# Kernel optimization log

Hardware: AMD Instinct MI355X
Metric: run time of the kernel (lower is better)

## Reference

```python
import jax, jax.numpy as jnp
import numpy as np

N_NODES = 100000
N_EDGES = 1600000
N_PAIRS = 200000
IN_C, HID_C, OUT_C = 128, 128, 64


def setup_inputs() -> dict:
    key = jax.random.key(0)
    ks = jax.random.split(key, 10)
    x = jax.random.normal(ks[0], (N_NODES, IN_C), dtype=jnp.float32)
    edge_index = jax.random.randint(ks[1], (2, N_EDGES), 0, N_NODES, dtype=jnp.int64)
    node_i = jax.random.randint(ks[2], (N_PAIRS,), 0, N_NODES, dtype=jnp.int64)
    node_j = jax.random.randint(ks[3], (N_PAIRS,), 0, N_NODES, dtype=jnp.int64)
    def glorot(k, fan_in, fan_out):
        s = jnp.sqrt(6.0 / (fan_in + fan_out))
        return jax.random.uniform(k, (fan_in, fan_out), jnp.float32, -s, s)
    W1 = glorot(ks[4], IN_C, HID_C)
    b1 = jnp.zeros((HID_C,), jnp.float32)
    W2 = glorot(ks[5], HID_C, HID_C)
    b2 = jnp.zeros((HID_C,), jnp.float32)
    W3 = glorot(ks[6], HID_C, OUT_C)
    b3 = jnp.zeros((OUT_C,), jnp.float32)
    return {"x": x, "edge_index": edge_index, "node_i": node_i, "node_j": node_j,
            "W1": W1, "b1": b1, "W2": W2, "b2": b2, "W3": W3, "b3": b3}


def _gcn_layer(h, src, dst, deg_inv, w_e, W, b):
    # h: [N, Cin] -> linear then symmetric-normalized aggregation (with self loops)
    h = h @ W  # [N, Cout]
    msg = h[src] * w_e[:, None]  # [E, Cout] gather + edge weight
    agg = jax.ops.segment_sum(msg, dst, num_segments=N_NODES)
    agg = agg + h * deg_inv[:, None]  # self-loop term: h_i / deg_i
    return agg + b


def reference(x, edge_index, node_i, node_j, W1, b1, W2, b2, W3, b3):
    src, dst = edge_index[0], edge_index[1]
    # GCN normalization with self loops: deg_i = 1 + in-degree
    ones = jnp.ones((N_EDGES,), jnp.float32)
    deg = jax.ops.segment_sum(ones, dst, num_segments=N_NODES) + 1.0
    dinv_sqrt = jax.lax.rsqrt(deg)
    deg_inv = 1.0 / deg
    w_e = dinv_sqrt[src] * dinv_sqrt[dst]  # [E]

    h = _gcn_layer(x, src, dst, deg_inv, w_e, W1, b1)
    h = jax.nn.relu(h)  # dropout is identity in eval mode
    h = _gcn_layer(h, src, dst, deg_inv, w_e, W2, b2)
    h = jax.nn.relu(h)
    h = _gcn_layer(h, src, dst, deg_inv, w_e, W3, b3)

    # dot-product link decode (decode_type=None)
    return jnp.sum(h[node_i] * h[node_j], axis=-1)  # [N_PAIRS]
```

## Files before the change

### kernel.cpp

```cpp
#include <hip/hip_runtime.h>

#define NN 100000
#define NNP 100032
#define NE 1600000
#define NP 200000
#define NBKT 782
#define BCAP 3072
#define BKB 4096

typedef short s16x8 __attribute__((ext_vector_type(8)));
typedef float f32x4 __attribute__((ext_vector_type(4)));

__device__ __forceinline__ unsigned short f2bf(float f) {
  unsigned int u = __float_as_uint(f);
  u += 0x7fffu + ((u >> 16) & 1u);
  return (unsigned short)(u >> 16);
}

__device__ __forceinline__ void upadd(uint u, float& lo, float& hi) {
  lo += __uint_as_float(u << 16);
  hi += __uint_as_float(u & 0xffff0000u);
}

template <int NT>
__device__ __forceinline__ void prepw_dev(const float* __restrict__ W,
                                          uint* __restrict__ Wt, int tid) {
  constexpr int COUT = NT * 16;
  if (tid >= 4 * NT * 64) return;
  int lane = tid & 63, comb = tid >> 6;
  int ks = comb / NT, tl = comb % NT;
  int q = lane >> 4, n = lane & 15;
  uint w[4];
#pragma unroll
  for (int jj = 0; jj < 4; ++jj) {
    int k0 = ks * 32 + q * 8 + 2 * jj;
    uint lo = f2bf(W[k0 * COUT + tl * 16 + n]);
    uint hi = f2bf(W[(k0 + 1) * COUT + tl * 16 + n]);
    w[jj] = lo | (hi << 16);
  }
  ((uint4*)Wt)[comb * 64 + lane] = make_uint4(w[0], w[1], w[2], w[3]);
}

__global__ __launch_bounds__(256) void k_setup(const float* __restrict__ W1,
                                               const float* __restrict__ W2,
                                               const float* __restrict__ W3,
                                               uint* __restrict__ Wt1,
                                               uint* __restrict__ Wt2,
                                               uint* __restrict__ Wt3,
                                               int* __restrict__ gcur) {
  int b = blockIdx.x, t = threadIdx.x;
  if (b < 4) {
    int i = b * 256 + t;
    if (i < 1024) gcur[i] = 0;
  } else if (b < 12) {
    prepw_dev<8>(W1, Wt1, (b - 4) * 256 + t);
  } else if (b < 20) {
    prepw_dev<8>(W2, Wt2, (b - 12) * 256 + t);
  } else {
    prepw_dev<4>(W3, Wt3, (b - 20) * 256 + t);
  }
}

__global__ __launch_bounds__(256) void k_bucket(const int* __restrict__ ei,
                                                int* __restrict__ gcur,
                                                int* __restrict__ aux) {
  __shared__ int cnt[1024];
  __shared__ int scn[1024];
  __shared__ int cur[1024];
  __shared__ int sc[256];
  __shared__ int sorted[BKB];
  __shared__ unsigned short sbkt[BKB];
  const int t = threadIdx.x;
  const int base = blockIdx.x * BKB;

  for (int i = t; i < 1024; i += 256) cnt[i] = 0;
  __syncthreads();

  int pk[16], bk[16];
#pragma unroll
  for (int i = 0; i < 16; ++i) {
    int e = base + t + 256 * i;
    if (e < NE) {
      int src = ei[e], dst = ei[NE + e];
      bk[i] = dst >> 7;
      pk[i] = src | ((dst & 127) << 17);
      atomicAdd(&cnt[bk[i]], 1);
    } else {
      bk[i] = -1;
    }
  }
  __syncthreads();

  int s0 = cnt[4 * t], s1 = cnt[4 * t + 1], s2 = cnt[4 * t + 2], s3 = cnt[4 * t + 3];
  int local = s0 + s1 + s2 + s3;
  sc[t] = local;
  __syncthreads();
  for (int off = 1; off < 256; off <<= 1) {
    int a = (t >= off) ? sc[t - off] : 0;
    __syncthreads();
    sc[t] += a;
    __syncthreads();
  }
  int b0 = sc[t] - local;
  scn[4 * t] = b0;
  scn[4 * t + 1] = b0 + s0;
  scn[4 * t + 2] = b0 + s0 + s1;
  scn[4 * t + 3] = b0 + s0 + s1 + s2;
  cur[4 * t] = scn[4 * t];
  cur[4 * t + 1] = scn[4 * t + 1];
  cur[4 * t + 2] = scn[4 * t + 2];
  cur[4 * t + 3] = scn[4 * t + 3];
  __syncthreads();
  const int tot = sc[255];

#pragma unroll
  for (int i = 0; i < 16; ++i) {
    if (bk[i] >= 0) {
      int pos = atomicAdd(&cur[bk[i]], 1);
      sorted[pos] = pk[i];
      sbkt[pos] = (unsigned short)bk[i];
    }
  }
  __syncthreads();

  for (int b = t; b < 1024; b += 256) {
    int c = cnt[b];
    if (c > 0) cur[b] = b * BCAP + atomicAdd(&gcur[b], c);
  }
  __syncthreads();

  for (int k = t; k < tot; k += 256) {
    int b = sbkt[k];
    aux[cur[b] + (k - scn[b])] = sorted[k];
  }
}

__global__ __launch_bounds__(256) void k_csr(const int* __restrict__ gcur,
                                             const int* __restrict__ aux,
                                             int* __restrict__ row_ptr,
                                             float* __restrict__ dinv,
                                             int* __restrict__ col) {
  __shared__ int red[256];
  __shared__ int c[128];
  __shared__ int cur[128];
  const int b = blockIdx.x, t = threadIdx.x;
  int p = 0;
  for (int i = t; i < b; i += 256) p += gcur[i];
  red[t] = p;
  if (t < 128) c[t] = 0;
  __syncthreads();
  for (int off = 128; off > 0; off >>= 1) {
    if (t < off) red[t] += red[t + off];
    __syncthreads();
  }
  const int base = red[0];
  const int m = gcur[b];
  const int* a = aux + (size_t)b * BCAP;
  __syncthreads();
  for (int k = t; k < m; k += 256) atomicAdd(&c[a[k] >> 17], 1);
  __syncthreads();
  int val = (t < 128) ? c[t] : 0;
  red[t] = val;
  __syncthreads();
  for (int off = 1; off < 128; off <<= 1) {
    int add = (t >= off && t < 128) ? red[t - off] : 0;
    __syncthreads();
    if (t < 128) red[t] += add;
    __syncthreads();
  }
  if (t < 128) {
    int excl = red[t] - val + base;
    int node = b * 128 + t;
    if (node < NN) {
      row_ptr[node] = excl;
      dinv[node] = rsqrtf((float)(val + 1));
      cur[t] = excl;
    }
  }
  if (b == NBKT - 1 && t == 0) row_ptr[NN] = base + m;
  __syncthreads();
  for (int k = t; k < m; k += 256) {
    int pk2 = a[k];
    int pos = atomicAdd(&cur[pk2 >> 17], 1);
    col[pos] = pk2 & 0x1FFFF;
  }
}

template <int COUT, bool AFP32>
__global__ __launch_bounds__(256) void k_gemm_mfma(const void* __restrict__ Av,
                                                   const uint* __restrict__ Wt,
                                                   const float* __restrict__ dinv,
                                                   unsigned short* __restrict__ T) {
  constexpr int NT = COUT / 16;
  __shared__ __align__(16) uint Wlds[4 * NT * 64 * 4];
  __shared__ __align__(16) unsigned short Obuf[64 * COUT];
  const int t = threadIdx.x;
  {
    const uint4* src = (const uint4*)Wt;
    uint4* dst = (uint4*)Wlds;
    for (int i = t; i < 4 * NT * 64; i += 256) dst[i] = src[i];
  }
  __syncthreads();

  const int wv = t >> 6, lane = t & 63;
  const int n = lane & 15, quad = lane >> 4;
  const int rbase = blockIdx.x * 64 + wv * 16;

  union AB { uint4 u; s16x8 s; };
  AB a[4];
  if constexpr (AFP32) {
    const float* A = (const float*)Av;
    int row = rbase + n;
    if (row >= NN) row = NN - 1;
    const float* ap = A + (size_t)row * 128;
#pragma unroll
    for (int ks = 0; ks < 4; ++ks) {
      float4 v0 = *(const float4*)(ap + ks * 32 + quad * 8);
      float4 v1 = *(const float4*)(ap + ks * 32 + quad * 8 + 4);
      a[ks].u.x = (uint)f2bf(v0.x) | ((uint)f2bf(v0.y) << 16);
      a[ks].u.y = (uint)f2bf(v0.z) | ((uint)f2bf(v0.w) << 16);
      a[ks].u.z = (uint)f2bf(v1.x) | ((uint)f2bf(v1.y) << 16);
      a[ks].u.w = (uint)f2bf(v1.z) | ((uint)f2bf(v1.w) << 16);
    }
  } else {
    const uint4* A = (const uint4*)Av;
    int row = rbase + n;
#pragma unroll
    for (int ks = 0; ks < 4; ++ks) a[ks].u = A[(size_t)row * 16 + ks * 4 + quad];
  }

  f32x4 acc[NT];
#pragma unroll
  for (int tl = 0; tl < NT; ++tl) acc[tl] = (f32x4){0.f, 0.f, 0.f, 0.f};

#pragma unroll
  for (int ks = 0; ks < 4; ++ks) {
#pragma unroll
    for (int tl = 0; tl < NT; ++tl) {
      AB b;
      b.u = *(const uint4*)&Wlds[((ks * NT + tl) * 64 + lane) * 4];
      acc[tl] = __builtin_amdgcn_mfma_f32_16x16x32_bf16(a[ks].s, b.s, acc[tl], 0, 0, 0);
    }
  }

  float4 dv = *(const float4*)(dinv + rbase + quad * 4);
  float dvv[4] = {dv.x, dv.y, dv.z, dv.w};
  unsigned short* ob = Obuf + wv * 16 * COUT;
#pragma unroll
  for (int tl = 0; tl < NT; ++tl)
#pragma unroll
    for (int r = 0; r < 4; ++r)
      ob[(quad * 4 + r) * COUT + tl * 16 + n] = f2bf(acc[tl][r] * dvv[r]);

  uint4* gdst = (uint4*)(T + (size_t)rbase * COUT);
  constexpr int ITER = COUT / 32;
#pragma unroll
  for (int i = 0; i < ITER; ++i) {
    int off16 = i * 64 + lane;
    int lrow = (off16 * 8) / COUT;
    uint4 v = make_uint4(0u, 0u, 0u, 0u);
    if (rbase + lrow < NN) v = *(const uint4*)&ob[off16 * 8];
    gdst[off16] = v;
  }
}

__global__ __launch_bounds__(256) void k_gather12(const int* __restrict__ row_ptr,
                                                  const int* __restrict__ col,
                                                  const uint4* __restrict__ T4,
                                                  const float* __restrict__ dinv,
                                                  const float* __restrict__ bias,
                                                  uint4* __restrict__ An) {
  int w = (blockIdx.x * 256 + threadIdx.x) >> 6;
  int lane = threadIdx.x & 63;
  if (w >= NN) return;
  int s = row_ptr[w], tend = row_ptr[w + 1];
  const int q = lane >> 4;
  const int cl = lane & 15;
  float acc[8] = {0.f, 0.f, 0.f, 0.f, 0.f, 0.f, 0.f, 0.f};
  if (q == 0) {
    uint4 u = T4[(size_t)w * 16 + cl];
    upadd(u.x, acc[0], acc[1]);
    upadd(u.y, acc[2], acc[3]);
    upadd(u.z, acc[4], acc[5]);
    upadd(u.w, acc[6], acc[7]);
  }
  const int d = tend - s;
  const int nfull = d >> 4;
  int e = s + q;
  for (int it = 0; it < nfull; ++it, e += 16) {
    int c0 = col[e], c1 = col[e + 4], c2 = col[e + 8], c3 = col[e + 12];
    uint4 v0 = T4[(size_t)c0 * 16 + cl];
    uint4 v1 = T4[(size_t)c1 * 16 + cl];
    uint4 v2 = T4[(size_t)c2 * 16 + cl];
    uint4 v3 = T4[(size_t)c3 * 16 + cl];
    upadd(v0.x, acc[0], acc[1]); upadd(v0.y, acc[2], acc[3]);
    upadd(v0.z, acc[4], acc[5]); upadd(v0.w, acc[6], acc[7]);
    upadd(v1.x, acc[0], acc[1]); upadd(v1.y, acc[2], acc[3]);
    upadd(v1.z, acc[4], acc[5]); upadd(v1.w, acc[6], acc[7]);
    upadd(v2.x, acc[0], acc[1]); upadd(v2.y, acc[2], acc[3]);
    upadd(v2.z, acc[4], acc[5]); upadd(v2.w, acc[6], acc[7]);
    upadd(v3.x, acc[0], acc[1]); upadd(v3.y, acc[2], acc[3]);
    upadd(v3.z, acc[4], acc[5]); upadd(v3.w, acc[6], acc[7]);
  }
  if (d & 15) {
    const int m = tend - 1;
    int i0 = e, i1 = e + 4, i2 = e + 8, i3 = e + 12;
    int c0 = col[min(i0, m)], c1 = col[min(i1, m)];
    int c2 = col[min(i2, m)], c3 = col[min(i3, m)];
    c0 = (i0 < tend) ? c0 : NN;
    c1 = (i1 < tend) ? c1 : NN;
    c2 = (i2 < tend) ? c2 : NN;
    c3 = (i3 < tend) ? c3 : NN;
    uint4 v0 = T4[(size_t)c0 * 16 + cl];
    uint4 v1 = T4[(size_t)c1 * 16 + cl];
    uint4 v2 = T4[(size_t)c2 * 16 + cl];
    uint4 v3 = T4[(size_t)c3 * 16 + cl];
    upadd(v0.x, acc[0], acc[1]); upadd(v0.y, acc[2], acc[3]);
    upadd(v0.z, acc[4], acc[5]); upadd(v0.w, acc[6], acc[7]);
    upadd(v1.x, acc[0], acc[1]); upadd(v1.y, acc[2], acc[3]);
    upadd(v1.z, acc[4], acc[5]); upadd(v1.w, acc[6], acc[7]);
    upadd(v2.x, acc[0], acc[1]); upadd(v2.y, acc[2], acc[3]);
    upadd(v2.z, acc[4], acc[5]); upadd(v2.w, acc[6], acc[7]);
    upadd(v3.x, acc[0], acc[1]); upadd(v3.y, acc[2], acc[3]);
    upadd(v3.z, acc[4], acc[5]); upadd(v3.w, acc[6], acc[7]);
  }
#pragma unroll
  for (int i = 0; i < 8; ++i) {
    acc[i] += __shfl_down(acc[i], 16, 64);
    acc[i] += __shfl_down(acc[i], 32, 64);
  }
  if (q == 0) {
    float4 b0 = *(const float4*)&bias[cl * 8];
    float4 b1 = *(const float4*)&bias[cl * 8 + 4];
    float dv = dinv[w];
    float r[8];
    r[0] = fmaxf(fmaf(dv, acc[0], b0.x), 0.f);
    r[1] = fmaxf(fmaf(dv, acc[1], b0.y), 0.f);
    r[2] = fmaxf(fmaf(dv, acc[2], b0.z), 0.f);
    r[3] = fmaxf(fmaf(dv, acc[3], b0.w), 0.f);
    r[4] = fmaxf(fmaf(dv, acc[4], b1.x), 0.f);
    r[5] = fmaxf(fmaf(dv, acc[5], b1.y), 0.f);
    r[6] = fmaxf(fmaf(dv, acc[6], b1.z), 0.f);
    r[7] = fmaxf(fmaf(dv, acc[7], b1.w), 0.f);
    uint4 o;
    o.x = (uint)f2bf(r[0]) | ((uint)f2bf(r[1]) << 16);
    o.y = (uint)f2bf(r[2]) | ((uint)f2bf(r[3]) << 16);
    o.z = (uint)f2bf(r[4]) | ((uint)f2bf(r[5]) << 16);
    o.w = (uint)f2bf(r[6]) | ((uint)f2bf(r[7]) << 16);
    An[(size_t)w * 16 + cl] = o;
  }
}

__global__ __launch_bounds__(256) void k_gather3(const int* __restrict__ row_ptr,
                                                 const int* __restrict__ col,
                                                 const uint4* __restrict__ T4,
                                                 uint4* __restrict__ G3) {
  int w = (blockIdx.x * 256 + threadIdx.x) >> 6;
  int lane = threadIdx.x & 63;
  if (w >= NN) return;
  int s = row_ptr[w], tend = row_ptr[w + 1];
  const int g = lane >> 3;
  const int cl = lane & 7;
  float acc[8] = {0.f, 0.f, 0.f, 0.f, 0.f, 0.f, 0.f, 0.f};
  if (g == 0) {
    uint4 u = T4[(size_t)w * 8 + cl];
    upadd(u.x, acc[0], acc[1]);
    upadd(u.y, acc[2], acc[3]);
    upadd(u.z, acc[4], acc[5]);
    upadd(u.w, acc[6], acc[7]);
  }
  const int d = tend - s;
  const int nfull = d >> 4;
  int e = s + g;
  for (int it = 0; it < nfull; ++it, e += 16) {
    int c0 = col[e], c1 = col[e + 8];
    uint4 v0 = T4[(size_t)c0 * 8 + cl];
    uint4 v1 = T4[(size_t)c1 * 8 + cl];
    upadd(v0.x, acc[0], acc[1]); upadd(v0.y, acc[2], acc[3]);
    upadd(v0.z, acc[4], acc[5]); upadd(v0.w, acc[6], acc[7]);
    upadd(v1.x, acc[0], acc[1]); upadd(v1.y, acc[2], acc[3]);
    upadd(v1.z, acc[4], acc[5]); upadd(v1.w, acc[6], acc[7]);
  }
  if (d & 15) {
    const int m = tend - 1;
    int i0 = e, i1 = e + 8;
    int c0 = col[min(i0, m)], c1 = col[min(i1, m)];
    c0 = (i0 < tend) ? c0 : NN;
    c1 = (i1 < tend) ? c1 : NN;
    uint4 v0 = T4[(size_t)c0 * 8 + cl];
    uint4 v1 = T4[(size_t)c1 * 8 + cl];
    upadd(v0.x, acc[0], acc[1]); upadd(v0.y, acc[2], acc[3]);
    upadd(v0.z, acc[4], acc[5]); upadd(v0.w, acc[6], acc[7]);
    upadd(v1.x, acc[0], acc[1]); upadd(v1.y, acc[2], acc[3]);
    upadd(v1.z, acc[4], acc[5]); upadd(v1.w, acc[6], acc[7]);
  }
#pragma unroll
  for (int i = 0; i < 8; ++i) {
    acc[i] += __shfl_down(acc[i], 8, 64);
    acc[i] += __shfl_down(acc[i], 16, 64);
    acc[i] += __shfl_down(acc[i], 32, 64);
  }
  if (g == 0) {
    uint4 o;
    o.x = (uint)f2bf(acc[0]) | ((uint)f2bf(acc[1]) << 16);
    o.y = (uint)f2bf(acc[2]) | ((uint)f2bf(acc[3]) << 16);
    o.z = (uint)f2bf(acc[4]) | ((uint)f2bf(acc[5]) << 16);
    o.w = (uint)f2bf(acc[6]) | ((uint)f2bf(acc[7]) << 16);
    G3[(size_t)w * 8 + cl] = o;
  }
}

__global__ __launch_bounds__(256) void k_decode(const int* __restrict__ ni,
                                                const int* __restrict__ nj,
                                                const uint2* __restrict__ G3,
                                                const float* __restrict__ dinv,
                                                const float* __restrict__ b3,
                                                float* __restrict__ out) {
  int p = blockIdx.x * 16 + (threadIdx.x >> 4);
  int cl = threadIdx.x & 15;
  int i = ni[p], j = nj[p];
  uint2 ui = G3[(size_t)i * 16 + cl];
  uint2 uj = G3[(size_t)j * 16 + cl];
  float4 bb = *(const float4*)&b3[cl * 4];
  float di = dinv[i], dj = dinv[j];
  float gi0 = __uint_as_float(ui.x << 16), gi1 = __uint_as_float(ui.x & 0xffff0000u);
  float gi2 = __uint_as_float(ui.y << 16), gi3 = __uint_as_float(ui.y & 0xffff0000u);
  float gj0 = __uint_as_float(uj.x << 16), gj1 = __uint_as_float(uj.x & 0xffff0000u);
  float gj2 = __uint_as_float(uj.y << 16), gj3 = __uint_as_float(uj.y & 0xffff0000u);
  float v = fmaf(di, gi0, bb.x) * fmaf(dj, gj0, bb.x) +
            fmaf(di, gi1, bb.y) * fmaf(dj, gj1, bb.y) +
            fmaf(di, gi2, bb.z) * fmaf(dj, gj2, bb.z) +
            fmaf(di, gi3, bb.w) * fmaf(dj, gj3, bb.w);
  v += __shfl_xor(v, 1, 64);
  v += __shfl_xor(v, 2, 64);
  v += __shfl_xor(v, 4, 64);
  v += __shfl_xor(v, 8, 64);
  if (cl == 0) out[p] = v;
}

extern "C" void kernel_launch(void* const* d_in, const int* in_sizes, int n_in,
                              void* d_out, int out_size, void* d_ws, size_t ws_size,
                              hipStream_t stream) {
  const float* x  = (const float*)d_in[0];
  const int*   ei = (const int*)d_in[1];
  const int*   ni = (const int*)d_in[2];
  const int*   nj = (const int*)d_in[3];
  const float* W1 = (const float*)d_in[4];
  const float* b1 = (const float*)d_in[5];
  const float* W2 = (const float*)d_in[6];
  const float* b2 = (const float*)d_in[7];
  const float* W3 = (const float*)d_in[8];
  const float* b3 = (const float*)d_in[9];
  float* out = (float*)d_out;

  float* dinv    = (float*)d_ws;
  int*   row_ptr = (int*)(dinv + 102400);
  int*   gcur    = row_ptr + 102400;
  int*   col     = gcur + 1024;
  uint*  Wt1     = (uint*)(col + NE);
  uint*  Wt2     = Wt1 + 8192;
  uint*  Wt3     = Wt2 + 8192;
  uint*  Tbf     = Wt3 + 4096;
  uint*  Abf     = Tbf + (size_t)NNP * 64;
  uint*  G3      = Abf + (size_t)NNP * 64;
  int*   aux     = (int*)G3;

  k_setup<<<24, 256, 0, stream>>>(W1, W2, W3, Wt1, Wt2, Wt3, gcur);
  k_bucket<<<(NE + BKB - 1) / BKB, 256, 0, stream>>>(ei, gcur, aux);
  k_csr<<<NBKT, 256, 0, stream>>>(gcur, aux, row_ptr, dinv, col);

  const int GB = NNP / 64;
  const int GATB = (NN * 64 + 255) / 256;

  k_gemm_mfma<128, true><<<GB, 256, 0, stream>>>(x, Wt1, dinv, (unsigned short*)Tbf);
  k_gather12<<<GATB, 256, 0, stream>>>(row_ptr, col, (const uint4*)Tbf, dinv, b1, (uint4*)Abf);
  k_gemm_mfma<128, false><<<GB, 256, 0, stream>>>(Abf, Wt2, dinv, (unsigned short*)Tbf);
  k_gather12<<<GATB, 256, 0, stream>>>(row_ptr, col, (const uint4*)Tbf, dinv, b2, (uint4*)Abf);
  k_gemm_mfma<64, false><<<GB, 256, 0, stream>>>(Abf, Wt3, dinv, (unsigned short*)Tbf);
  k_gather3<<<GATB, 256, 0, stream>>>(row_ptr, col, (const uint4*)Tbf, (uint4*)G3);
  k_decode<<<NP / 16, 256, 0, stream>>>(ni, nj, (const uint2*)G3, dinv, b3, out);
}
```

Measured before the change: 339.6 us.

## Fuse neighbor aggregation with the next layer's MFMA GEMM per 16-node tile

```diff
diff --git a/kernel.cpp b/kernel.cpp
--- a/kernel.cpp
+++ b/kernel.cpp
@@ -186,12 +186,11 @@
   }
 }
 
-template <int COUT, bool AFP32>
-__global__ __launch_bounds__(256) void k_gemm_mfma(const void* __restrict__ Av,
-                                                   const uint* __restrict__ Wt,
-                                                   const float* __restrict__ dinv,
-                                                   unsigned short* __restrict__ T) {
-  constexpr int NT = COUT / 16;
+__global__ __launch_bounds__(256) void k_gemm1(const float* __restrict__ A,
+                                               const uint* __restrict__ Wt,
+                                               const float* __restrict__ dinv,
+                                               unsigned short* __restrict__ T) {
+  constexpr int NT = 8, COUT = 128;
   __shared__ __align__(16) uint Wlds[4 * NT * 64 * 4];
   __shared__ __align__(16) unsigned short Obuf[64 * COUT];
   const int t = threadIdx.x;
@@ -208,8 +207,7 @@
 
   union AB { uint4 u; s16x8 s; };
   AB a[4];
-  if constexpr (AFP32) {
-    const float* A = (const float*)Av;
+  {
     int row = rbase + n;
     if (row >= NN) row = NN - 1;
     const float* ap = A + (size_t)row * 128;
@@ -222,11 +220,6 @@
       a[ks].u.z = (uint)f2bf(v1.x) | ((uint)f2bf(v1.y) << 16);
       a[ks].u.w = (uint)f2bf(v1.z) | ((uint)f2bf(v1.w) << 16);
     }
-  } else {
-    const uint4* A = (const uint4*)Av;
-    int row = rbase + n;
-#pragma unroll
-    for (int ks = 0; ks < 4; ++ks) a[ks].u = A[(size_t)row * 16 + ks * 4 + quad];
   }
 
   f32x4 acc[NT];
@@ -253,9 +246,8 @@
       ob[(quad * 4 + r) * COUT + tl * 16 + n] = f2bf(acc[tl][r] * dvv[r]);
 
   uint4* gdst = (uint4*)(T + (size_t)rbase * COUT);
-  constexpr int ITER = COUT / 32;
-#pragma unroll
-  for (int i = 0; i < ITER; ++i) {
+#pragma unroll
+  for (int i = 0; i < 4; ++i) {
     int off16 = i * 64 + lane;
     int lrow = (off16 * 8) / COUT;
     uint4 v = make_uint4(0u, 0u, 0u, 0u);
@@ -264,90 +256,147 @@
   }
 }
 
-__global__ __launch_bounds__(256) void k_gather12(const int* __restrict__ row_ptr,
-                                                  const int* __restrict__ col,
-                                                  const uint4* __restrict__ T4,
-                                                  const float* __restrict__ dinv,
-                                                  const float* __restrict__ bias,
-                                                  uint4* __restrict__ An) {
-  int w = (blockIdx.x * 256 + threadIdx.x) >> 6;
-  int lane = threadIdx.x & 63;
-  if (w >= NN) return;
-  int s = row_ptr[w], tend = row_ptr[w + 1];
-  const int q = lane >> 4;
-  const int cl = lane & 15;
-  float acc[8] = {0.f, 0.f, 0.f, 0.f, 0.f, 0.f, 0.f, 0.f};
-  if (q == 0) {
-    uint4 u = T4[(size_t)w * 16 + cl];
-    upadd(u.x, acc[0], acc[1]);
-    upadd(u.y, acc[2], acc[3]);
-    upadd(u.z, acc[4], acc[5]);
-    upadd(u.w, acc[6], acc[7]);
-  }
-  const int d = tend - s;
-  const int nfull = d >> 4;
-  int e = s + q;
-  for (int it = 0; it < nfull; ++it, e += 16) {
-    int c0 = col[e], c1 = col[e + 4], c2 = col[e + 8], c3 = col[e + 12];
-    uint4 v0 = T4[(size_t)c0 * 16 + cl];
-    uint4 v1 = T4[(size_t)c1 * 16 + cl];
-    uint4 v2 = T4[(size_t)c2 * 16 + cl];
-    uint4 v3 = T4[(size_t)c3 * 16 + cl];
-    upadd(v0.x, acc[0], acc[1]); upadd(v0.y, acc[2], acc[3]);
-    upadd(v0.z, acc[4], acc[5]); upadd(v0.w, acc[6], acc[7]);
-    upadd(v1.x, acc[0], acc[1]); upadd(v1.y, acc[2], acc[3]);
-    upadd(v1.z, acc[4], acc[5]); upadd(v1.w, acc[6], acc[7]);
-    upadd(v2.x, acc[0], acc[1]); upadd(v2.y, acc[2], acc[3]);
-    upadd(v2.z, acc[4], acc[5]); upadd(v2.w, acc[6], acc[7]);
-    upadd(v3.x, acc[0], acc[1]); upadd(v3.y, acc[2], acc[3]);
-    upadd(v3.z, acc[4], acc[5]); upadd(v3.w, acc[6], acc[7]);
-  }
-  if (d & 15) {
-    const int m = tend - 1;
-    int i0 = e, i1 = e + 4, i2 = e + 8, i3 = e + 12;
-    int c0 = col[min(i0, m)], c1 = col[min(i1, m)];
-    int c2 = col[min(i2, m)], c3 = col[min(i3, m)];
-    c0 = (i0 < tend) ? c0 : NN;
-    c1 = (i1 < tend) ? c1 : NN;
-    c2 = (i2 < tend) ? c2 : NN;
-    c3 = (i3 < tend) ? c3 : NN;
-    uint4 v0 = T4[(size_t)c0 * 16 + cl];
-    uint4 v1 = T4[(size_t)c1 * 16 + cl];
-    uint4 v2 = T4[(size_t)c2 * 16 + cl];
-    uint4 v3 = T4[(size_t)c3 * 16 + cl];
-    upadd(v0.x, acc[0], acc[1]); upadd(v0.y, acc[2], acc[3]);
-    upadd(v0.z, acc[4], acc[5]); upadd(v0.w, acc[6], acc[7]);
-    upadd(v1.x, acc[0], acc[1]); upadd(v1.y, acc[2], acc[3]);
-    upadd(v1.z, acc[4], acc[5]); upadd(v1.w, acc[6], acc[7]);
-    upadd(v2.x, acc[0], acc[1]); upadd(v2.y, acc[2], acc[3]);
-    upadd(v2.z, acc[4], acc[5]); upadd(v2.w, acc[6], acc[7]);
-    upadd(v3.x, acc[0], acc[1]); upadd(v3.y, acc[2], acc[3]);
-    upadd(v3.z, acc[4], acc[5]); upadd(v3.w, acc[6], acc[7]);
-  }
-#pragma unroll
-  for (int i = 0; i < 8; ++i) {
-    acc[i] += __shfl_down(acc[i], 16, 64);
-    acc[i] += __shfl_down(acc[i], 32, 64);
-  }
-  if (q == 0) {
-    float4 b0 = *(const float4*)&bias[cl * 8];
-    float4 b1 = *(const float4*)&bias[cl * 8 + 4];
-    float dv = dinv[w];
-    float r[8];
-    r[0] = fmaxf(fmaf(dv, acc[0], b0.x), 0.f);
-    r[1] = fmaxf(fmaf(dv, acc[1], b0.y), 0.f);
-    r[2] = fmaxf(fmaf(dv, acc[2], b0.z), 0.f);
-    r[3] = fmaxf(fmaf(dv, acc[3], b0.w), 0.f);
-    r[4] = fmaxf(fmaf(dv, acc[4], b1.x), 0.f);
-    r[5] = fmaxf(fmaf(dv, acc[5], b1.y), 0.f);
-    r[6] = fmaxf(fmaf(dv, acc[6], b1.z), 0.f);
-    r[7] = fmaxf(fmaf(dv, acc[7], b1.w), 0.f);
-    uint4 o;
-    o.x = (uint)f2bf(r[0]) | ((uint)f2bf(r[1]) << 16);
-    o.y = (uint)f2bf(r[2]) | ((uint)f2bf(r[3]) << 16);
-    o.z = (uint)f2bf(r[4]) | ((uint)f2bf(r[5]) << 16);
-    o.w = (uint)f2bf(r[6]) | ((uint)f2bf(r[7]) << 16);
-    An[(size_t)w * 16 + cl] = o;
+template <int COUT>
+__global__ __launch_bounds__(256) void k_gg(const int* __restrict__ row_ptr,
+                                            const int* __restrict__ col,
+                                            const uint4* __restrict__ T4,
+                                            const float* __restrict__ dinv,
+                                            const float* __restrict__ bias,
+                                            const uint4* __restrict__ Wt,
+                                            unsigned short* __restrict__ Tout) {
+  constexpr int NT = COUT / 16;
+  constexpr int TLW = NT / 4;
+  constexpr int OSTR = COUT + 8;
+  __shared__ __align__(16) uint4 Alds[16 * 17];
+  const int t = threadIdx.x, wv = t >> 6, lane = t & 63;
+  const int nbase = blockIdx.x * 16;
+  const int q = lane >> 4, cl = lane & 15;
+
+#pragma unroll 1
+  for (int i = 0; i < 4; ++i) {
+    const int node = nbase + wv * 4 + i;
+    int s = 0, tend = 0;
+    if (node < NN) { s = row_ptr[node]; tend = row_ptr[node + 1]; }
+    float acc[8] = {0.f, 0.f, 0.f, 0.f, 0.f, 0.f, 0.f, 0.f};
+    if (q == 0) {
+      uint4 u = T4[(size_t)node * 16 + cl];
+      upadd(u.x, acc[0], acc[1]);
+      upadd(u.y, acc[2], acc[3]);
+      upadd(u.z, acc[4], acc[5]);
+      upadd(u.w, acc[6], acc[7]);
+    }
+    const int d = tend - s;
+    const int nfull = d >> 4;
+    int e = s + q;
+    for (int it = 0; it < nfull; ++it, e += 16) {
+      int c0 = col[e], c1 = col[e + 4], c2 = col[e + 8], c3 = col[e + 12];
+      uint4 v0 = T4[(size_t)c0 * 16 + cl];
+      uint4 v1 = T4[(size_t)c1 * 16 + cl];
+      uint4 v2 = T4[(size_t)c2 * 16 + cl];
+      uint4 v3 = T4[(size_t)c3 * 16 + cl];
+      upadd(v0.x, acc[0], acc[1]); upadd(v0.y, acc[2], acc[3]);
+      upadd(v0.z, acc[4], acc[5]); upadd(v0.w, acc[6], acc[7]);
+      upadd(v1.x, acc[0], acc[1]); upadd(v1.y, acc[2], acc[3]);
+      upadd(v1.z, acc[4], acc[5]); upadd(v1.w, acc[6], acc[7]);
+      upadd(v2.x, acc[0], acc[1]); upadd(v2.y, acc[2], acc[3]);
+      upadd(v2.z, acc[4], acc[5]); upadd(v2.w, acc[6], acc[7]);
+      upadd(v3.x, acc[0], acc[1]); upadd(v3.y, acc[2], acc[3]);
+      upadd(v3.z, acc[4], acc[5]); upadd(v3.w, acc[6], acc[7]);
+    }
+    if (d & 15) {
+      const int m = tend - 1;
+      int i0 = e, i1 = e + 4, i2 = e + 8, i3 = e + 12;
+      int c0 = col[min(i0, m)], c1 = col[min(i1, m)];
+      int c2 = col[min(i2, m)], c3 = col[min(i3, m)];
+      c0 = (i0 < tend) ? c0 : NN;
+      c1 = (i1 < tend) ? c1 : NN;
+      c2 = (i2 < tend) ? c2 : NN;
+      c3 = (i3 < tend) ? c3 : NN;
+      uint4 v0 = T4[(size_t)c0 * 16 + cl];
+      uint4 v1 = T4[(size_t)c1 * 16 + cl];
+      uint4 v2 = T4[(size_t)c2 * 16 + cl];
+      uint4 v3 = T4[(size_t)c3 * 16 + cl];
+      upadd(v0.x, acc[0], acc[1]); upadd(v0.y, acc[2], acc[3]);
+      upadd(v0.z, acc[4], acc[5]); upadd(v0.w, acc[6], acc[7]);
+      upadd(v1.x, acc[0], acc[1]); upadd(v1.y, acc[2], acc[3]);
+      upadd(v1.z, acc[4], acc[5]); upadd(v1.w, acc[6], acc[7]);
+      upadd(v2.x, acc[0], acc[1]); upadd(v2.y, acc[2], acc[3]);
+      upadd(v2.z, acc[4], acc[5]); upadd(v2.w, acc[6], acc[7]);
+      upadd(v3.x, acc[0], acc[1]); upadd(v3.y, acc[2], acc[3]);
+      upadd(v3.z, acc[4], acc[5]); upadd(v3.w, acc[6], acc[7]);
+    }
+#pragma unroll
+    for (int k = 0; k < 8; ++k) {
+      acc[k] += __shfl_down(acc[k], 16, 64);
+      acc[k] += __shfl_down(acc[k], 32, 64);
+    }
+    if (q == 0) {
+      float4 b0 = *(const float4*)&bias[cl * 8];
+      float4 b1 = *(const float4*)&bias[cl * 8 + 4];
+      float dv = dinv[node];
+      float r[8];
+      r[0] = fmaxf(fmaf(dv, acc[0], b0.x), 0.f);
+      r[1] = fmaxf(fmaf(dv, acc[1], b0.y), 0.f);
+      r[2] = fmaxf(fmaf(dv, acc[2], b0.z), 0.f);
+      r[3] = fmaxf(fmaf(dv, acc[3], b0.w), 0.f);
+      r[4] = fmaxf(fmaf(dv, acc[4], b1.x), 0.f);
+      r[5] = fmaxf(fmaf(dv, acc[5], b1.y), 0.f);
+      r[6] = fmaxf(fmaf(dv, acc[6], b1.z), 0.f);
+      r[7] = fmaxf(fmaf(dv, acc[7], b1.w), 0.f);
+      uint4 o;
+      o.x = (uint)f2bf(r[0]) | ((uint)f2bf(r[1]) << 16);
+      o.y = (uint)f2bf(r[2]) | ((uint)f2bf(r[3]) << 16);
+      o.z = (uint)f2bf(r[4]) | ((uint)f2bf(r[5]) << 16);
+      o.w = (uint)f2bf(r[6]) | ((uint)f2bf(r[7]) << 16);
+      Alds[(wv * 4 + i) * 17 + cl] = o;
+    }
+  }
+  __syncthreads();
+
+  const int n = lane & 15, quad = lane >> 4;
+  union AB { uint4 u; s16x8 s; };
+  AB a[4];
+#pragma unroll
+  for (int ks = 0; ks < 4; ++ks) a[ks].u = Alds[n * 17 + ks * 4 + quad];
+  f32x4 acc2[TLW];
+#pragma unroll
+  for (int j = 0; j < TLW; ++j) acc2[j] = (f32x4){0.f, 0.f, 0.f, 0.f};
+#pragma unroll
+  for (int ks = 0; ks < 4; ++ks) {
+#pragma unroll
+    for (int j = 0; j < TLW; ++j) {
+      int tl = wv * TLW + j;
+      AB b;
+      b.u = Wt[(ks * NT + tl) * 64 + lane];
+      acc2[j] = __builtin_amdgcn_mfma_f32_16x16x32_bf16(a[ks].s, b.s, acc2[j], 0, 0, 0);
+    }
+  }
+  __syncthreads();
+
+  unsigned short* Obuf = (unsigned short*)Alds;
+  float4 dv4 = *(const float4*)(dinv + nbase + quad * 4);
+  float dvv[4] = {dv4.x, dv4.y, dv4.z, dv4.w};
+#pragma unroll
+  for (int j = 0; j < TLW; ++j) {
+    int tl = wv * TLW + j;
+#pragma unroll
+    for (int r = 0; r < 4; ++r)
+      Obuf[(quad * 4 + r) * OSTR + tl * 16 + n] = f2bf(acc2[j][r] * dvv[r]);
+  }
+  __syncthreads();
+
+  if constexpr (COUT == 128) {
+    int row = t >> 4, c16 = t & 15;
+    uint4 v = make_uint4(0u, 0u, 0u, 0u);
+    if (nbase + row < NN) v = *(const uint4*)&Obuf[row * OSTR + c16 * 8];
+    ((uint4*)(Tout + (size_t)nbase * COUT))[row * 16 + c16] = v;
+  } else {
+    if (t < 128) {
+      int row = t >> 3, c16 = t & 7;
+      uint4 v = make_uint4(0u, 0u, 0u, 0u);
+      if (nbase + row < NN) v = *(const uint4*)&Obuf[row * OSTR + c16 * 8];
+      ((uint4*)(Tout + (size_t)nbase * COUT))[row * 8 + c16] = v;
+    }
   }
 }
 
@@ -461,8 +510,8 @@
   uint*  Wt2     = Wt1 + 8192;
   uint*  Wt3     = Wt2 + 8192;
   uint*  Tbf     = Wt3 + 4096;
-  uint*  Abf     = Tbf + (size_t)NNP * 64;
-  uint*  G3      = Abf + (size_t)NNP * 64;
+  uint*  T2      = Tbf + (size_t)NNP * 64;
+  uint*  G3      = T2 + (size_t)NNP * 64;
   int*   aux     = (int*)G3;
 
   k_setup<<<24, 256, 0, stream>>>(W1, W2, W3, Wt1, Wt2, Wt3, gcur);
@@ -470,13 +519,14 @@
   k_csr<<<NBKT, 256, 0, stream>>>(gcur, aux, row_ptr, dinv, col);
 
   const int GB = NNP / 64;
+  const int FB = NNP / 16;
   const int GATB = (NN * 64 + 255) / 256;
 
-  k_gemm_mfma<128, true><<<GB, 256, 0, stream>>>(x, Wt1, dinv, (unsigned short*)Tbf);
-  k_gather12<<<GATB, 256, 0, stream>>>(row_ptr, col, (const uint4*)Tbf, dinv, b1, (uint4*)Abf);
-  k_gemm_mfma<128, false><<<GB, 256, 0, stream>>>(Abf, Wt2, dinv, (unsigned short*)Tbf);
-  k_gather12<<<GATB, 256, 0, stream>>>(row_ptr, col, (const uint4*)Tbf, dinv, b2, (uint4*)Abf);
-  k_gemm_mfma<64, false><<<GB, 256, 0, stream>>>(Abf, Wt3, dinv, (unsigned short*)Tbf);
+  k_gemm1<<<GB, 256, 0, stream>>>(x, Wt1, dinv, (unsigned short*)Tbf);
+  k_gg<128><<<FB, 256, 0, stream>>>(row_ptr, col, (const uint4*)Tbf, dinv, b1,
+                                    (const uint4*)Wt2, (unsigned short*)T2);
+  k_gg<64><<<FB, 256, 0, stream>>>(row_ptr, col, (const uint4*)T2, dinv, b2,
+                                   (const uint4*)Wt3, (unsigned short*)Tbf);
   k_gather3<<<GATB, 256, 0, stream>>>(row_ptr, col, (const uint4*)Tbf, (uint4*)G3);
   k_decode<<<NP / 16, 256, 0, stream>>>(ni, nj, (const uint2*)G3, dinv, b3, out);
 }
```

New measurement: 330.2 us. -2.8%, faster.
